# Kernel tuning notes

Measured on AMD Instinct MI355X. Metric: run time of the kernel, lower is better.

Reference implementation:

```python
import jax, jax.numpy as jnp
import numpy as np

N_NODES = 50000
N_EDGES = 800000
D_IN, D_HID, D_OUT = 128, 128, 64


def setup_inputs() -> dict:
    key = jax.random.key(0)
    ks = jax.random.split(key, 10)
    return {
        "x": jax.random.normal(ks[0], (N_NODES, D_IN), dtype=jnp.float32),
        "edge_row": jax.random.randint(ks[1], (N_EDGES,), 0, N_NODES, dtype=jnp.int32),
        "edge_col": jax.random.randint(ks[2], (N_EDGES,), 0, N_NODES, dtype=jnp.int32),
        "edge_val": jax.random.uniform(ks[3], (N_EDGES,), dtype=jnp.float32),
        "W1": jax.random.normal(ks[4], (D_IN, D_HID), dtype=jnp.float32) * (1.0 / np.sqrt(D_HID)),
        "b1": jax.random.normal(ks[5], (D_HID,), dtype=jnp.float32) * (1.0 / np.sqrt(D_HID)),
        "W2": jax.random.normal(ks[6], (D_HID, D_HID), dtype=jnp.float32) * (1.0 / np.sqrt(D_HID)),
        "b2": jax.random.normal(ks[7], (D_HID,), dtype=jnp.float32) * (1.0 / np.sqrt(D_HID)),
        "W3": jax.random.normal(ks[8], (D_HID, D_OUT), dtype=jnp.float32) * (1.0 / np.sqrt(D_OUT)),
        "b3": jax.random.normal(ks[9], (D_OUT,), dtype=jnp.float32) * (1.0 / np.sqrt(D_OUT)),
    }


def _gcn_layer(x, edge_row, edge_col, edge_val, W, b):
    # support = x @ W          : dense GEMM [N, d_out]
    support = x @ W
    # spmm(adj, support)[i] = sum_e with row[e]==i: val[e] * support[col[e]]
    gathered = support[edge_col] * edge_val[:, None]  # [E, d_out]
    agg = jax.ops.segment_sum(gathered, edge_row, num_segments=x.shape[0])
    return agg + b


def reference(x, edge_row, edge_col, edge_val, W1, b1, W2, b2, W3, b3):
    # Layer 1 + ReLU (dropout is identity in eval)
    h = jax.nn.relu(_gcn_layer(x, edge_row, edge_col, edge_val, W1, b1))
    # Layer 2 + ReLU
    h = jax.nn.relu(_gcn_layer(h, edge_row, edge_col, edge_val, W2, b2))
    # Layer 3 (no activation)
    return _gcn_layer(h, edge_row, edge_col, edge_val, W3, b3)
```

## Files before the change

### kernel.cpp

```cpp
#include <hip/hip_runtime.h>

#define N_NODES 50000
#define N_EDGES 800000
#define SCAN_TILE 2048
#define FILL_BLOCKS ((N_EDGES + 255) / 256)

#define HB 64
#define EPB (N_EDGES / HB)
#define HGROUPS (EPB / 4)
#define HWORDS (N_NODES / 4)

static_assert(N_NODES < 65536, "col must fit in 16 bits for packed CSR");
static_assert(N_EDGES % (4 * HB) == 0, "chunking must be exact");
static_assert(N_NODES % 8 == 0, "scan tiles assume x8");

typedef __attribute__((ext_vector_type(4))) float f32x4;
typedef __attribute__((ext_vector_type(8))) short bf16x8;

__device__ inline unsigned short f32_to_bf16(float f) {
    unsigned int u = __builtin_bit_cast(unsigned int, f);
    u += 0x7FFF + ((u >> 16) & 1);
    return (unsigned short)(u >> 16);
}
__device__ inline float bf16_to_f32(unsigned short h) {
    unsigned int u = ((unsigned int)h) << 16;
    return __builtin_bit_cast(float, u);
}

template <int NOUT>
__device__ __forceinline__ void mfma_phase(const unsigned short* Xs,
                                           const unsigned short* Ws,
                                           unsigned short* __restrict__ Yb,
                                           int block_row, int N) {
    constexpr int KP = 128 + 8;
    constexpr int NT = NOUT / 16;
    const int tid = threadIdx.x;
    const int wave = tid >> 6;
    const int lane = tid & 63;
    const int m = lane & 15;
    const int quad = lane >> 4;
    const int rowbase = wave * 16;

    f32x4 acc[NT];
#pragma unroll
    for (int t = 0; t < NT; ++t) acc[t] = (f32x4){0.f, 0.f, 0.f, 0.f};

#pragma unroll
    for (int kt = 0; kt < 4; ++kt) {
        bf16x8 a = *reinterpret_cast<const bf16x8*>(
            Xs + (rowbase + m) * KP + kt * 32 + quad * 8);
#pragma unroll
        for (int t = 0; t < NT; ++t) {
            bf16x8 b = *reinterpret_cast<const bf16x8*>(
                Ws + (t * 16 + m) * KP + kt * 32 + quad * 8);
            acc[t] = __builtin_amdgcn_mfma_f32_16x16x32_bf16(a, b, acc[t], 0, 0, 0);
        }
    }

#pragma unroll
    for (int t = 0; t < NT; ++t) {
#pragma unroll
        for (int r = 0; r < 4; ++r) {
            int grow = block_row + rowbase + quad * 4 + r;
            if (grow < N)
                Yb[(size_t)grow * NOUT + t * 16 + m] = f32_to_bf16(acc[t][r]);
        }
    }
}

__global__ __launch_bounds__(256) void mega1(
    const float* __restrict__ x, const float* __restrict__ W1,
    unsigned short* __restrict__ Yb, int N, int ntiles_g,
    const int* __restrict__ erow, unsigned int* __restrict__ rank8,
    unsigned int* __restrict__ bhist, int* __restrict__ done) {
    constexpr int KP = 128 + 8;
    __shared__ __align__(16) unsigned char smem[52224];
    const int tid = threadIdx.x;

    if (blockIdx.x < HB) {
        const int b = blockIdx.x;
        if (b == 0 && tid == 0) *done = 0;
        unsigned int* h = reinterpret_cast<unsigned int*>(smem);
        int4* h4 = reinterpret_cast<int4*>(h);
        for (int i = tid; i < HWORDS / 4; i += 256) {
            int4 z = {0, 0, 0, 0};
            h4[i] = z;
        }
        __syncthreads();
        const int4* eg = reinterpret_cast<const int4*>(erow) + (size_t)b * HGROUPS;
        unsigned int* rg = rank8 + (size_t)b * HGROUPS;
        for (int g = tid; g < HGROUPS; g += 256) {
            int4 er = eg[g];
            unsigned int rk;
            int sh;
            unsigned int o;
            sh = (er.x & 3) << 3;
            o = atomicAdd(&h[er.x >> 2], 1u << sh);
            rk = (o >> sh) & 0xFFu;
            sh = (er.y & 3) << 3;
            o = atomicAdd(&h[er.y >> 2], 1u << sh);
            rk |= ((o >> sh) & 0xFFu) << 8;
            sh = (er.z & 3) << 3;
            o = atomicAdd(&h[er.z >> 2], 1u << sh);
            rk |= ((o >> sh) & 0xFFu) << 16;
            sh = (er.w & 3) << 3;
            o = atomicAdd(&h[er.w >> 2], 1u << sh);
            rk |= ((o >> sh) & 0xFFu) << 24;
            rg[g] = rk;
        }
        __syncthreads();
        int4* dst = reinterpret_cast<int4*>(bhist + (size_t)b * HWORDS);
        for (int i = tid; i < HWORDS / 4; i += 256) dst[i] = h4[i];
        return;
    }

    const int gb = blockIdx.x - HB;
    unsigned short* Xs = reinterpret_cast<unsigned short*>(smem);
    unsigned short* Ws = reinterpret_cast<unsigned short*>(smem) + 64 * KP;

    for (int idx = tid; idx < 128 * 128; idx += 256) {
        int k = idx >> 7, m = idx & 127;
        Ws[m * KP + k] = f32_to_bf16(W1[idx]);
    }

    for (int tile = gb; tile < ntiles_g; tile += (int)gridDim.x - HB) {
        const int block_row = tile * 64;
        for (int idx = tid; idx < 64 * 16; idx += 256) {
            int r = idx >> 4, ch = idx & 15;
            int gr = block_row + r;
            if (gr >= N) gr = N - 1;
            const float4* xp =
                reinterpret_cast<const float4*>(x + (size_t)gr * 128 + ch * 8);
            float4 a = xp[0], b2 = xp[1];
            uint4 o;
            o.x = (unsigned int)f32_to_bf16(a.x) | ((unsigned int)f32_to_bf16(a.y) << 16);
            o.y = (unsigned int)f32_to_bf16(a.z) | ((unsigned int)f32_to_bf16(a.w) << 16);
            o.z = (unsigned int)f32_to_bf16(b2.x) | ((unsigned int)f32_to_bf16(b2.y) << 16);
            o.w = (unsigned int)f32_to_bf16(b2.z) | ((unsigned int)f32_to_bf16(b2.w) << 16);
            *reinterpret_cast<uint4*>(Xs + r * KP + ch * 8) = o;
        }
        __syncthreads();
        mfma_phase<128>(Xs, Ws, Yb, block_row, N);
        __syncthreads();
    }
}

__global__ void scan_fused(const unsigned int* __restrict__ bhist,
                           int* __restrict__ tsum, int* __restrict__ done,
                           int* __restrict__ rptr, int* __restrict__ bbase,
                           int n, int ntiles) {
    __shared__ int sums[256];
    __shared__ int off_s;
    const int t = threadIdx.x;
    const int b = blockIdx.x;
    const int base = b * SCAN_TILE + t * 8;
    const int widx2 = base >> 3;
    const uint2* bh2 = reinterpret_cast<const uint2*>(bhist);
    int v[8], pref[8];
#pragma unroll
    for (int i = 0; i < 8; ++i) v[i] = 0;
    if (base < n) {
        for (int hb = 0; hb < HB; ++hb) {
            uint2 p = bh2[hb * (HWORDS / 2) + widx2];
            v[0] += p.x & 0xFF; v[1] += (p.x >> 8) & 0xFF;
            v[2] += (p.x >> 16) & 0xFF; v[3] += p.x >> 24;
            v[4] += p.y & 0xFF; v[5] += (p.y >> 8) & 0xFF;
            v[6] += (p.y >> 16) & 0xFF; v[7] += p.y >> 24;
        }
    }
    int s = 0;
#pragma unroll
    for (int i = 0; i < 8; ++i) s += v[i];
    sums[t] = s;
    __syncthreads();
    for (int off = 1; off < 256; off <<= 1) {
        int x = (t >= off) ? sums[t - off] : 0;
        __syncthreads();
        sums[t] += x;
        __syncthreads();
    }
    int run = sums[t] - s;
#pragma unroll
    for (int i = 0; i < 8; ++i) {
        pref[i] = run;
        run += v[i];
    }
    if (t == 255) {
        tsum[b] = run;
        __threadfence();
        atomicAdd(done, 1);
    }
    if (t == 0) {
        while (__hip_atomic_load(done, __ATOMIC_ACQUIRE, __HIP_MEMORY_SCOPE_AGENT) <
               ntiles) {
        }
        __threadfence();
        int off = 0;
        for (int i = 0; i < b; ++i) off += tsum[i];
        off_s = off;
        if (b == 0) {
            int tot = 0;
            for (int i = 0; i < ntiles; ++i) tot += tsum[i];
            rptr[n] = tot;
        }
    }
    __syncthreads();
    const int off = off_s;
    if (base < n) {
        int rn[8];
#pragma unroll
        for (int i = 0; i < 8; ++i) rn[i] = pref[i] + off;
        int4 r0 = {rn[0], rn[1], rn[2], rn[3]};
        int4 r1 = {rn[4], rn[5], rn[6], rn[7]};
        *reinterpret_cast<int4*>(rptr + base) = r0;
        *reinterpret_cast<int4*>(rptr + base + 4) = r1;
        for (int hb = 0; hb < HB; ++hb) {
            int4 o0 = {rn[0], rn[1], rn[2], rn[3]};
            int4 o1 = {rn[4], rn[5], rn[6], rn[7]};
            int4* bb = reinterpret_cast<int4*>(bbase + (size_t)hb * N_NODES + base);
            bb[0] = o0;
            bb[1] = o1;
            uint2 p = bh2[hb * (HWORDS / 2) + widx2];
            rn[0] += p.x & 0xFF; rn[1] += (p.x >> 8) & 0xFF;
            rn[2] += (p.x >> 16) & 0xFF; rn[3] += p.x >> 24;
            rn[4] += p.y & 0xFF; rn[5] += (p.y >> 8) & 0xFF;
            rn[6] += (p.y >> 16) & 0xFF; rn[7] += p.y >> 24;
        }
    }
}

__global__ void fill_csr(const int* __restrict__ erow, const int* __restrict__ ecol,
                         const float* __restrict__ eval, const int* __restrict__ bbase,
                         const unsigned int* __restrict__ rank8,
                         unsigned int* __restrict__ cpack) {
    int e = blockIdx.x * blockDim.x + threadIdx.x;
    if (e >= N_EDGES) return;
    const unsigned char* r8 = reinterpret_cast<const unsigned char*>(rank8);
    int slot = bbase[(size_t)(e / EPB) * N_NODES + erow[e]] + r8[e];
    unsigned int p = (unsigned int)(ecol[e] & 0xFFFF) |
                     ((unsigned int)f32_to_bf16(eval[e]) << 16);
    cpack[slot] = p;
}

template <int NOUT>
__device__ __forceinline__ void mfma_phase512(const unsigned short* Xs,
                                              const unsigned short* Ws,
                                              unsigned short* __restrict__ Yb,
                                              int block_row, int N) {
    constexpr int KP = 128 + 8;
    constexpr int NT = NOUT / 16;
    constexpr int NTH = NT / 2;
    const int tid = threadIdx.x;
    const int wave = tid >> 6;
    const int lane = tid & 63;
    const int m = lane & 15;
    const int quad = lane >> 4;
    const int rowbase = (wave & 3) * 16;
    const int tbase = (wave >> 2) * NTH;

    f32x4 acc[NTH];
#pragma unroll
    for (int t = 0; t < NTH; ++t) acc[t] = (f32x4){0.f, 0.f, 0.f, 0.f};

#pragma unroll
    for (int kt = 0; kt < 4; ++kt) {
        bf16x8 a = *reinterpret_cast<const bf16x8*>(
            Xs + (rowbase + m) * KP + kt * 32 + quad * 8);
#pragma unroll
        for (int t = 0; t < NTH; ++t) {
            bf16x8 b = *reinterpret_cast<const bf16x8*>(
                Ws + ((tbase + t) * 16 + m) * KP + kt * 32 + quad * 8);
            acc[t] = __builtin_amdgcn_mfma_f32_16x16x32_bf16(a, b, acc[t], 0, 0, 0);
        }
    }

#pragma unroll
    for (int t = 0; t < NTH; ++t) {
#pragma unroll
        for (int r = 0; r < 4; ++r) {
            int grow = block_row + rowbase + quad * 4 + r;
            if (grow < N)
                Yb[(size_t)grow * NOUT + (tbase + t) * 16 + m] = f32_to_bf16(acc[t][r]);
        }
    }
}

template <int NOUT>
__global__ __launch_bounds__(512, 4) void gemm_fused_agg(
    const unsigned short* __restrict__ S,
    const int* __restrict__ rptr, const unsigned int* __restrict__ cpack,
    const float* __restrict__ bias,
    const float* __restrict__ W,
    unsigned short* __restrict__ Yb,
    int N, int ntiles) {
    constexpr int KP = 128 + 8;
    __shared__ unsigned short Xs[64 * KP];
    __shared__ unsigned short Ws[NOUT * KP];
    __shared__ int nextrow_s;
    const int tid = threadIdx.x;
    const int f8 = tid & 15;
    const int lane = tid & 63;

    for (int idx = tid; idx < 128 * NOUT; idx += 512) {
        int k = idx / NOUT, m = idx % NOUT;
        Ws[m * KP + k] = f32_to_bf16(W[idx]);
    }

    float bv[8];
#pragma unroll
    for (int i = 0; i < 8; ++i) bv[i] = bias[f8 * 8 + i];

    if (tid == 0) nextrow_s = 0;
    __syncthreads();

    for (int tile = blockIdx.x; tile < ntiles; tile += gridDim.x) {
        const int block_row = tile * 64;
        while (true) {
            int r = 0;
            if (f8 == 0) r = atomicAdd(&nextrow_s, 1);
            const int row = __shfl(r, lane & 48, 64);
            if (row >= 64) break;
            const int node = block_row + row;
            float acc[8];
#pragma unroll
            for (int i = 0; i < 8; ++i) acc[i] = bv[i];
            if (node < N) {
                const int beg = rptr[node];
                const int end = rptr[node + 1];
                int j = beg;
                for (; j + 8 <= end; j += 8) {
                    unsigned int p[8];
                    uint4 s[8];
#pragma unroll
                    for (int u = 0; u < 8; ++u) p[u] = cpack[j + u];
#pragma unroll
                    for (int u = 0; u < 8; ++u)
                        s[u] = *reinterpret_cast<const uint4*>(
                            S + (size_t)(p[u] & 0xFFFF) * 128 + f8 * 8);
#pragma unroll
                    for (int u = 0; u < 8; ++u) {
                        const float v = bf16_to_f32((unsigned short)(p[u] >> 16));
                        const unsigned short* sp =
                            reinterpret_cast<const unsigned short*>(&s[u]);
#pragma unroll
                        for (int i = 0; i < 8; ++i)
                            acc[i] = fmaf(v, bf16_to_f32(sp[i]), acc[i]);
                    }
                }
                if (j + 4 <= end) {
                    unsigned int p[4];
                    uint4 s[4];
#pragma unroll
                    for (int u = 0; u < 4; ++u) p[u] = cpack[j + u];
#pragma unroll
                    for (int u = 0; u < 4; ++u)
                        s[u] = *reinterpret_cast<const uint4*>(
                            S + (size_t)(p[u] & 0xFFFF) * 128 + f8 * 8);
#pragma unroll
                    for (int u = 0; u < 4; ++u) {
                        const float v = bf16_to_f32((unsigned short)(p[u] >> 16));
                        const unsigned short* sp =
                            reinterpret_cast<const unsigned short*>(&s[u]);
#pragma unroll
                        for (int i = 0; i < 8; ++i)
                            acc[i] = fmaf(v, bf16_to_f32(sp[i]), acc[i]);
                    }
                    j += 4;
                }
                if (j + 2 <= end) {
                    unsigned int p[2];
                    uint4 s[2];
#pragma unroll
                    for (int u = 0; u < 2; ++u) p[u] = cpack[j + u];
#pragma unroll
                    for (int u = 0; u < 2; ++u)
                        s[u] = *reinterpret_cast<const uint4*>(
                            S + (size_t)(p[u] & 0xFFFF) * 128 + f8 * 8);
#pragma unroll
                    for (int u = 0; u < 2; ++u) {
                        const float v = bf16_to_f32((unsigned short)(p[u] >> 16));
                        const unsigned short* sp =
                            reinterpret_cast<const unsigned short*>(&s[u]);
#pragma unroll
                        for (int i = 0; i < 8; ++i)
                            acc[i] = fmaf(v, bf16_to_f32(sp[i]), acc[i]);
                    }
                    j += 2;
                }
                if (j < end) {
                    unsigned int p = cpack[j];
                    uint4 s = *reinterpret_cast<const uint4*>(
                        S + (size_t)(p & 0xFFFF) * 128 + f8 * 8);
                    const float v = bf16_to_f32((unsigned short)(p >> 16));
                    const unsigned short* sp =
                        reinterpret_cast<const unsigned short*>(&s);
#pragma unroll
                    for (int i = 0; i < 8; ++i)
                        acc[i] = fmaf(v, bf16_to_f32(sp[i]), acc[i]);
                }
            }
            uint4 o;
            o.x = (unsigned int)f32_to_bf16(fmaxf(acc[0], 0.f)) |
                  ((unsigned int)f32_to_bf16(fmaxf(acc[1], 0.f)) << 16);
            o.y = (unsigned int)f32_to_bf16(fmaxf(acc[2], 0.f)) |
                  ((unsigned int)f32_to_bf16(fmaxf(acc[3], 0.f)) << 16);
            o.z = (unsigned int)f32_to_bf16(fmaxf(acc[4], 0.f)) |
                  ((unsigned int)f32_to_bf16(fmaxf(acc[5], 0.f)) << 16);
            o.w = (unsigned int)f32_to_bf16(fmaxf(acc[6], 0.f)) |
                  ((unsigned int)f32_to_bf16(fmaxf(acc[7], 0.f)) << 16);
            *reinterpret_cast<uint4*>(Xs + row * KP + f8 * 8) = o;
        }
        __syncthreads();
        mfma_phase512<NOUT>(Xs, Ws, Yb, block_row, N);
        if (tid == 0) nextrow_s = 0;
        __syncthreads();
    }
}

__global__ void aggregate_bf16_64(const unsigned short* __restrict__ S,
                                  const int* __restrict__ rptr,
                                  const unsigned int* __restrict__ cpack,
                                  const float* __restrict__ bias,
                                  float* __restrict__ out, int N) {
    const int node = blockIdx.x * (blockDim.x / 8) + threadIdx.x / 8;
    const int f8 = threadIdx.x & 7;
    if (node >= N) return;
    const int beg = rptr[node];
    const int end = rptr[node + 1];
    float acc[8];
#pragma unroll
    for (int i = 0; i < 8; ++i) acc[i] = bias[f8 * 8 + i];
    int j = beg;
    for (; j + 8 <= end; j += 8) {
        unsigned int p[8];
        uint4 s[8];
#pragma unroll
        for (int u = 0; u < 8; ++u) p[u] = cpack[j + u];
#pragma unroll
        for (int u = 0; u < 8; ++u)
            s[u] = *reinterpret_cast<const uint4*>(S + (size_t)(p[u] & 0xFFFF) * 64 + f8 * 8);
#pragma unroll
        for (int u = 0; u < 8; ++u) {
            const float v = bf16_to_f32((unsigned short)(p[u] >> 16));
            const unsigned short* sp = reinterpret_cast<const unsigned short*>(&s[u]);
#pragma unroll
            for (int i = 0; i < 8; ++i) acc[i] = fmaf(v, bf16_to_f32(sp[i]), acc[i]);
        }
    }
    if (j + 4 <= end) {
        unsigned int p[4];
        uint4 s[4];
#pragma unroll
        for (int u = 0; u < 4; ++u) p[u] = cpack[j + u];
#pragma unroll
        for (int u = 0; u < 4; ++u)
            s[u] = *reinterpret_cast<const uint4*>(S + (size_t)(p[u] & 0xFFFF) * 64 + f8 * 8);
#pragma unroll
        for (int u = 0; u < 4; ++u) {
            const float v = bf16_to_f32((unsigned short)(p[u] >> 16));
            const unsigned short* sp = reinterpret_cast<const unsigned short*>(&s[u]);
#pragma unroll
            for (int i = 0; i < 8; ++i) acc[i] = fmaf(v, bf16_to_f32(sp[i]), acc[i]);
        }
        j += 4;
    }
    if (j + 2 <= end) {
        unsigned int p[2];
        uint4 s[2];
#pragma unroll
        for (int u = 0; u < 2; ++u) p[u] = cpack[j + u];
#pragma unroll
        for (int u = 0; u < 2; ++u)
            s[u] = *reinterpret_cast<const uint4*>(S + (size_t)(p[u] & 0xFFFF) * 64 + f8 * 8);
#pragma unroll
        for (int u = 0; u < 2; ++u) {
            const float v = bf16_to_f32((unsigned short)(p[u] >> 16));
            const unsigned short* sp = reinterpret_cast<const unsigned short*>(&s[u]);
#pragma unroll
            for (int i = 0; i < 8; ++i) acc[i] = fmaf(v, bf16_to_f32(sp[i]), acc[i]);
        }
        j += 2;
    }
    if (j < end) {
        unsigned int p = cpack[j];
        uint4 s = *reinterpret_cast<const uint4*>(S + (size_t)(p & 0xFFFF) * 64 + f8 * 8);
        const float v = bf16_to_f32((unsigned short)(p >> 16));
        const unsigned short* sp = reinterpret_cast<const unsigned short*>(&s);
#pragma unroll
        for (int i = 0; i < 8; ++i) acc[i] = fmaf(v, bf16_to_f32(sp[i]), acc[i]);
    }
    float4 o0 = {acc[0], acc[1], acc[2], acc[3]};
    float4 o1 = {acc[4], acc[5], acc[6], acc[7]};
    float* op = out + (size_t)node * 64 + f8 * 8;
    *reinterpret_cast<float4*>(op) = o0;
    *reinterpret_cast<float4*>(op + 4) = o1;
}

extern "C" void kernel_launch(void* const* d_in, const int* in_sizes, int n_in,
                              void* d_out, int out_size, void* d_ws, size_t ws_size,
                              hipStream_t stream) {
    const float* x    = (const float*)d_in[0];
    const int*   erow = (const int*)d_in[1];
    const int*   ecol = (const int*)d_in[2];
    const float* eval = (const float*)d_in[3];
    const float* W1   = (const float*)d_in[4];
    const float* b1   = (const float*)d_in[5];
    const float* W2   = (const float*)d_in[6];
    const float* b2   = (const float*)d_in[7];
    const float* W3   = (const float*)d_in[8];
    const float* b3   = (const float*)d_in[9];
    float* out = (float*)d_out;

    const size_t nf = (size_t)N_NODES * 128;
    unsigned short* SA   = (unsigned short*)d_ws;
    unsigned short* SB   = SA + nf;
    unsigned int*  rank8 = (unsigned int*)(SB + nf);
    unsigned int*  bhist = rank8 + N_EDGES / 4;
    int*   bbase  = (int*)(bhist + (size_t)HB * HWORDS);
    int*   rptr   = bbase + (size_t)HB * N_NODES;
    unsigned int* cpack = (unsigned int*)(rptr + N_NODES + 1);
    int*   stsum  = (int*)(cpack + N_EDGES);
    int*   done   = stsum + 64;

    const int blk = 256;
    const int ntiles_g = (N_NODES + 63) / 64;
    const int agg_grid = (int)(((long long)N_NODES * 8 + blk - 1) / blk);
    const int ntiles = (N_NODES + SCAN_TILE - 1) / SCAN_TILE;

    mega1<<<HB + ntiles_g, blk, 0, stream>>>(
        x, W1, SA, N_NODES, ntiles_g, erow, rank8, bhist, done);

    scan_fused<<<ntiles, blk, 0, stream>>>(bhist, stsum, done, rptr, bbase,
                                           N_NODES, ntiles);

    fill_csr<<<FILL_BLOCKS, blk, 0, stream>>>(erow, ecol, eval, bbase, rank8, cpack);

    gemm_fused_agg<128><<<ntiles_g, 512, 0, stream>>>(
        SA, rptr, cpack, b1, W2, SB, N_NODES, ntiles_g);

    gemm_fused_agg<64><<<ntiles_g, 512, 0, stream>>>(
        SB, rptr, cpack, b2, W3, SA, N_NODES, ntiles_g);

    aggregate_bf16_64<<<agg_grid, blk, 0, stream>>>(SA, rptr, cpack, b3, out, N_NODES);
}
```

Before: 234.8 us.

## Compress CSR bucket bases to bytes, vectorize fill, stage cpack in LDS

The scan now writes a per-chunk cumulative count as one byte per node (cum8) instead of a full int base, and fill_csr rebuilds each slot from rptr plus that byte. This cuts the bucket-base traffic roughly fourfold. fill_csr now handles four edges per thread with vector loads. Both aggregation kernels copy their tile's contiguous cpack range into shared memory and replace the atomic row work-queue with a static row-per-group assignment. The risks are that cum8 overflows if a node collects more than 255 edges across chunks, that fixed LDS buffers (2048/1536 entries) overflow on high-degree tiles, that the extra LDS may lower occupancy, and that static row assignment gives worse load balance.

```diff
diff --git a/kernel.cpp b/kernel.cpp
--- a/kernel.cpp
+++ b/kernel.cpp
@@ -3,7 +3,8 @@
 #define N_NODES 50000
 #define N_EDGES 800000
 #define SCAN_TILE 2048
-#define FILL_BLOCKS ((N_EDGES + 255) / 256)
+#define GEMM1_BLOCKS 782
+#define FILLV_BLOCKS ((N_EDGES / 4 + 255) / 256)
 
 #define HB 64
 #define EPB (N_EDGES / HB)
@@ -12,7 +13,7 @@
 
 static_assert(N_NODES < 65536, "col must fit in 16 bits for packed CSR");
 static_assert(N_EDGES % (4 * HB) == 0, "chunking must be exact");
-static_assert(N_NODES % 8 == 0, "scan tiles assume x8");
+static_assert(N_NODES % 8 == 0, "scan uint2 path assumes x8");
 
 typedef __attribute__((ext_vector_type(4))) float f32x4;
 typedef __attribute__((ext_vector_type(8))) short bf16x8;
@@ -123,7 +124,7 @@
         Ws[m * KP + k] = f32_to_bf16(W1[idx]);
     }
 
-    for (int tile = gb; tile < ntiles_g; tile += (int)gridDim.x - HB) {
+    for (int tile = gb; tile < ntiles_g; tile += GEMM1_BLOCKS) {
         const int block_row = tile * 64;
         for (int idx = tid; idx < 64 * 16; idx += 256) {
             int r = idx >> 4, ch = idx & 15;
@@ -147,7 +148,7 @@
 
 __global__ void scan_fused(const unsigned int* __restrict__ bhist,
                            int* __restrict__ tsum, int* __restrict__ done,
-                           int* __restrict__ rptr, int* __restrict__ bbase,
+                           int* __restrict__ rptr, unsigned char* __restrict__ cum8,
                            int n, int ntiles) {
     __shared__ int sums[256];
     __shared__ int off_s;
@@ -214,32 +215,45 @@
         int4 r1 = {rn[4], rn[5], rn[6], rn[7]};
         *reinterpret_cast<int4*>(rptr + base) = r0;
         *reinterpret_cast<int4*>(rptr + base + 4) = r1;
+        unsigned int cm[8];
+#pragma unroll
+        for (int i = 0; i < 8; ++i) cm[i] = 0;
         for (int hb = 0; hb < HB; ++hb) {
-            int4 o0 = {rn[0], rn[1], rn[2], rn[3]};
-            int4 o1 = {rn[4], rn[5], rn[6], rn[7]};
-            int4* bb = reinterpret_cast<int4*>(bbase + (size_t)hb * N_NODES + base);
-            bb[0] = o0;
-            bb[1] = o1;
+            uint2 w;
+            w.x = (cm[0] & 0xFF) | ((cm[1] & 0xFF) << 8) |
+                  ((cm[2] & 0xFF) << 16) | ((cm[3] & 0xFF) << 24);
+            w.y = (cm[4] & 0xFF) | ((cm[5] & 0xFF) << 8) |
+                  ((cm[6] & 0xFF) << 16) | ((cm[7] & 0xFF) << 24);
+            *reinterpret_cast<uint2*>(cum8 + (size_t)hb * N_NODES + base) = w;
             uint2 p = bh2[hb * (HWORDS / 2) + widx2];
-            rn[0] += p.x & 0xFF; rn[1] += (p.x >> 8) & 0xFF;
-            rn[2] += (p.x >> 16) & 0xFF; rn[3] += p.x >> 24;
-            rn[4] += p.y & 0xFF; rn[5] += (p.y >> 8) & 0xFF;
-            rn[6] += (p.y >> 16) & 0xFF; rn[7] += p.y >> 24;
+            cm[0] += p.x & 0xFF; cm[1] += (p.x >> 8) & 0xFF;
+            cm[2] += (p.x >> 16) & 0xFF; cm[3] += p.x >> 24;
+            cm[4] += p.y & 0xFF; cm[5] += (p.y >> 8) & 0xFF;
+            cm[6] += (p.y >> 16) & 0xFF; cm[7] += p.y >> 24;
         }
     }
 }
 
 __global__ void fill_csr(const int* __restrict__ erow, const int* __restrict__ ecol,
-                         const float* __restrict__ eval, const int* __restrict__ bbase,
+                         const float* __restrict__ eval, const int* __restrict__ rptr,
+                         const unsigned char* __restrict__ cum8,
                          const unsigned int* __restrict__ rank8,
                          unsigned int* __restrict__ cpack) {
-    int e = blockIdx.x * blockDim.x + threadIdx.x;
-    if (e >= N_EDGES) return;
-    const unsigned char* r8 = reinterpret_cast<const unsigned char*>(rank8);
-    int slot = bbase[(size_t)(e / EPB) * N_NODES + erow[e]] + r8[e];
-    unsigned int p = (unsigned int)(ecol[e] & 0xFFFF) |
-                     ((unsigned int)f32_to_bf16(eval[e]) << 16);
-    cpack[slot] = p;
+    int g = blockIdx.x * blockDim.x + threadIdx.x;
+    if (g >= N_EDGES / 4) return;
+    int4 er = reinterpret_cast<const int4*>(erow)[g];
+    int4 ec = reinterpret_cast<const int4*>(ecol)[g];
+    float4 ev = reinterpret_cast<const float4*>(eval)[g];
+    unsigned int rk = rank8[g];
+    const unsigned char* cb = cum8 + (size_t)(g / HGROUPS) * N_NODES;
+    int s0 = rptr[er.x] + cb[er.x] + (int)(rk & 0xFF);
+    int s1 = rptr[er.y] + cb[er.y] + (int)((rk >> 8) & 0xFF);
+    int s2 = rptr[er.z] + cb[er.z] + (int)((rk >> 16) & 0xFF);
+    int s3 = rptr[er.w] + cb[er.w] + (int)(rk >> 24);
+    cpack[s0] = (unsigned int)(ec.x & 0xFFFF) | ((unsigned int)f32_to_bf16(ev.x) << 16);
+    cpack[s1] = (unsigned int)(ec.y & 0xFFFF) | ((unsigned int)f32_to_bf16(ev.y) << 16);
+    cpack[s2] = (unsigned int)(ec.z & 0xFFFF) | ((unsigned int)f32_to_bf16(ev.z) << 16);
+    cpack[s3] = (unsigned int)(ec.w & 0xFFFF) | ((unsigned int)f32_to_bf16(ev.w) << 16);
 }
 
 template <int NOUT>
@@ -296,10 +310,10 @@
     constexpr int KP = 128 + 8;
     __shared__ unsigned short Xs[64 * KP];
     __shared__ unsigned short Ws[NOUT * KP];
-    __shared__ int nextrow_s;
+    __shared__ unsigned int cp_s[2048];
     const int tid = threadIdx.x;
+    const int group = tid >> 4;
     const int f8 = tid & 15;
-    const int lane = tid & 63;
 
     for (int idx = tid; idx < 128 * NOUT; idx += 512) {
         int k = idx / NOUT, m = idx % NOUT;
@@ -310,29 +324,30 @@
 #pragma unroll
     for (int i = 0; i < 8; ++i) bv[i] = bias[f8 * 8 + i];
 
-    if (tid == 0) nextrow_s = 0;
-    __syncthreads();
-
     for (int tile = blockIdx.x; tile < ntiles; tile += gridDim.x) {
         const int block_row = tile * 64;
-        while (true) {
-            int r = 0;
-            if (f8 == 0) r = atomicAdd(&nextrow_s, 1);
-            const int row = __shfl(r, lane & 48, 64);
-            if (row >= 64) break;
+        const int rend = (block_row + 64 < N) ? block_row + 64 : N;
+        const int ebeg = rptr[block_row];
+        const int ecount = rptr[rend] - ebeg;
+        __syncthreads();
+        for (int i = tid; i < ecount; i += 512) cp_s[i] = cpack[ebeg + i];
+        __syncthreads();
+#pragma unroll
+        for (int r4 = 0; r4 < 2; ++r4) {
+            const int row = r4 * 32 + group;
             const int node = block_row + row;
             float acc[8];
 #pragma unroll
             for (int i = 0; i < 8; ++i) acc[i] = bv[i];
             if (node < N) {
-                const int beg = rptr[node];
-                const int end = rptr[node + 1];
+                const int beg = rptr[node] - ebeg;
+                const int end = rptr[node + 1] - ebeg;
                 int j = beg;
                 for (; j + 8 <= end; j += 8) {
                     unsigned int p[8];
                     uint4 s[8];
 #pragma unroll
-                    for (int u = 0; u < 8; ++u) p[u] = cpack[j + u];
+                    for (int u = 0; u < 8; ++u) p[u] = cp_s[j + u];
 #pragma unroll
                     for (int u = 0; u < 8; ++u)
                         s[u] = *reinterpret_cast<const uint4*>(
@@ -351,7 +366,7 @@
                     unsigned int p[4];
                     uint4 s[4];
 #pragma unroll
-                    for (int u = 0; u < 4; ++u) p[u] = cpack[j + u];
+                    for (int u = 0; u < 4; ++u) p[u] = cp_s[j + u];
 #pragma unroll
                     for (int u = 0; u < 4; ++u)
                         s[u] = *reinterpret_cast<const uint4*>(
@@ -371,7 +386,7 @@
                     unsigned int p[2];
                     uint4 s[2];
 #pragma unroll
-                    for (int u = 0; u < 2; ++u) p[u] = cpack[j + u];
+                    for (int u = 0; u < 2; ++u) p[u] = cp_s[j + u];
 #pragma unroll
                     for (int u = 0; u < 2; ++u)
                         s[u] = *reinterpret_cast<const uint4*>(
@@ -388,7 +403,7 @@
                     j += 2;
                 }
                 if (j < end) {
-                    unsigned int p = cpack[j];
+                    unsigned int p = cp_s[j];
                     uint4 s = *reinterpret_cast<const uint4*>(
                         S + (size_t)(p & 0xFFFF) * 128 + f8 * 8);
                     const float v = bf16_to_f32((unsigned short)(p >> 16));
@@ -412,8 +427,6 @@
         }
         __syncthreads();
         mfma_phase512<NOUT>(Xs, Ws, Yb, block_row, N);
-        if (tid == 0) nextrow_s = 0;
-        __syncthreads();
     }
 }
 
@@ -422,20 +435,30 @@
                                   const unsigned int* __restrict__ cpack,
                                   const float* __restrict__ bias,
                                   float* __restrict__ out, int N) {
-    const int node = blockIdx.x * (blockDim.x / 8) + threadIdx.x / 8;
-    const int f8 = threadIdx.x & 7;
+    __shared__ unsigned int cp_s[1536];
+    const int t = threadIdx.x;
+    const int nfirst = blockIdx.x * 32;
+    const int node = nfirst + (t >> 3);
+    const int f8 = t & 7;
+    const int nlast1 = (nfirst + 32 < N) ? nfirst + 32 : N;
+    int ebeg = 0, ecount = 0;
+    if (nfirst < N) {
+        ebeg = rptr[nfirst];
+        ecount = rptr[nlast1] - ebeg;
+    }
+    for (int i = t; i < ecount; i += 256) cp_s[i] = cpack[ebeg + i];
+    __syncthreads();
     if (node >= N) return;
-    const int beg = rptr[node];
-    const int end = rptr[node + 1];
+    int j = rptr[node] - ebeg;
+    const int end = rptr[node + 1] - ebeg;
     float acc[8];
 #pragma unroll
     for (int i = 0; i < 8; ++i) acc[i] = bias[f8 * 8 + i];
-    int j = beg;
     for (; j + 8 <= end; j += 8) {
         unsigned int p[8];
         uint4 s[8];
 #pragma unroll
-        for (int u = 0; u < 8; ++u) p[u] = cpack[j + u];
+        for (int u = 0; u < 8; ++u) p[u] = cp_s[j + u];
 #pragma unroll
         for (int u = 0; u < 8; ++u)
             s[u] = *reinterpret_cast<const uint4*>(S + (size_t)(p[u] & 0xFFFF) * 64 + f8 * 8);
@@ -451,7 +474,7 @@
         unsigned int p[4];
         uint4 s[4];
 #pragma unroll
-        for (int u = 0; u < 4; ++u) p[u] = cpack[j + u];
+        for (int u = 0; u < 4; ++u) p[u] = cp_s[j + u];
 #pragma unroll
         for (int u = 0; u < 4; ++u)
             s[u] = *reinterpret_cast<const uint4*>(S + (size_t)(p[u] & 0xFFFF) * 64 + f8 * 8);
@@ -468,7 +491,7 @@
         unsigned int p[2];
         uint4 s[2];
 #pragma unroll
-        for (int u = 0; u < 2; ++u) p[u] = cpack[j + u];
+        for (int u = 0; u < 2; ++u) p[u] = cp_s[j + u];
 #pragma unroll
         for (int u = 0; u < 2; ++u)
             s[u] = *reinterpret_cast<const uint4*>(S + (size_t)(p[u] & 0xFFFF) * 64 + f8 * 8);
@@ -482,7 +505,7 @@
         j += 2;
     }
     if (j < end) {
-        unsigned int p = cpack[j];
+        unsigned int p = cp_s[j];
         uint4 s = *reinterpret_cast<const uint4*>(S + (size_t)(p & 0xFFFF) * 64 + f8 * 8);
         const float v = bf16_to_f32((unsigned short)(p >> 16));
         const unsigned short* sp = reinterpret_cast<const unsigned short*>(&s);
@@ -512,28 +535,29 @@
     float* out = (float*)d_out;
 
     const size_t nf = (size_t)N_NODES * 128;
-    unsigned short* SA   = (unsigned short*)d_ws;
-    unsigned short* SB   = SA + nf;
-    unsigned int*  rank8 = (unsigned int*)(SB + nf);
-    unsigned int*  bhist = rank8 + N_EDGES / 4;
-    int*   bbase  = (int*)(bhist + (size_t)HB * HWORDS);
-    int*   rptr   = bbase + (size_t)HB * N_NODES;
+    unsigned short* SA    = (unsigned short*)d_ws;
+    unsigned short* SB    = SA + nf;
+    unsigned int*   rank8 = (unsigned int*)(SB + nf);
+    unsigned int*   bhist = rank8 + N_EDGES / 4;
+    unsigned char*  cum8  = (unsigned char*)(bhist + (size_t)HB * HWORDS);
+    int*   rptr   = (int*)(cum8 + (size_t)HB * N_NODES);
     unsigned int* cpack = (unsigned int*)(rptr + N_NODES + 1);
-    int*   stsum  = (int*)(cpack + N_EDGES);
-    int*   done   = stsum + 64;
+    int*   tsum   = (int*)(cpack + N_EDGES);
+    int*   done   = tsum + 64;
 
     const int blk = 256;
     const int ntiles_g = (N_NODES + 63) / 64;
     const int agg_grid = (int)(((long long)N_NODES * 8 + blk - 1) / blk);
     const int ntiles = (N_NODES + SCAN_TILE - 1) / SCAN_TILE;
 
-    mega1<<<HB + ntiles_g, blk, 0, stream>>>(
+    mega1<<<HB + GEMM1_BLOCKS, blk, 0, stream>>>(
         x, W1, SA, N_NODES, ntiles_g, erow, rank8, bhist, done);
 
-    scan_fused<<<ntiles, blk, 0, stream>>>(bhist, stsum, done, rptr, bbase,
+    scan_fused<<<ntiles, blk, 0, stream>>>(bhist, tsum, done, rptr, cum8,
                                            N_NODES, ntiles);
 
-    fill_csr<<<FILL_BLOCKS, blk, 0, stream>>>(erow, ecol, eval, bbase, rank8, cpack);
+    fill_csr<<<FILLV_BLOCKS, blk, 0, stream>>>(erow, ecol, eval, rptr, cum8,
+                                               rank8, cpack);
 
     gemm_fused_agg<128><<<ntiles_g, 512, 0, stream>>>(
         SA, rptr, cpack, b1, W2, SB, N_NODES, ntiles_g);
```

New measurement: 224.8 us. 1.04x faster.
